# Kernel tuning notes

Hardware: AMD Instinct MI355X
Metric: run time of the kernel (lower is better)

## Reference

```python
import jax, jax.numpy as jnp
import numpy as np

B, N, F = 512, 2048, 64
T = 4            # number of atom types
H1, H2 = 64, 32  # hidden widths; final layer outputs 1 (per-atom energy)


def setup_inputs() -> dict:
    key = jax.random.key(0)
    ks = jax.random.split(key, 8)
    x = jax.random.normal(ks[0], (B, N, F), dtype=jnp.float32)
    atomic_numbers = jax.random.randint(ks[1], (N,), 0, T)
    s = 0.05
    # Per-type MLP parameters, stacked over the type axis (torch Linear layout: [out, in]).
    w0 = jax.random.normal(ks[2], (T, H1, F), dtype=jnp.float32) * s
    b0 = jax.random.normal(ks[3], (T, H1), dtype=jnp.float32) * s
    w1 = jax.random.normal(ks[4], (T, H2, H1), dtype=jnp.float32) * s
    b1 = jax.random.normal(ks[5], (T, H2), dtype=jnp.float32) * s
    w2 = jax.random.normal(ks[6], (T, 1, H2), dtype=jnp.float32) * s
    b2 = jax.random.normal(ks[7], (T, 1), dtype=jnp.float32) * s
    return {"x": x, "atomic_numbers": atomic_numbers,
            "w0": w0, "b0": b0, "w1": w1, "b1": b1, "w2": w2, "b2": b2}


def reference(x, atomic_numbers, w0, b0, w1, b1, w2, b2):
    # Behler-Parrinello: route each atom through the MLP of its atom type,
    # then sum per-atom energies over atoms.  The torch version gathers atoms
    # by type, runs each type's MLP, and scatters back; here we evaluate all
    # T type-MLPs batched over the type axis and select with a one-hot mask
    # (identical math, jit-friendly, no data-dependent shapes).
    onehot = jax.nn.one_hot(atomic_numbers, w0.shape[0], dtype=x.dtype)  # [N, T]
    h = jax.nn.silu(jnp.einsum('bnf,thf->tbnh', x, w0) + b0[:, None, None, :])   # [T,B,N,H1]
    h = jax.nn.silu(jnp.einsum('tbnh,tgh->tbng', h, w1) + b1[:, None, None, :])  # [T,B,N,H2]
    e = jnp.einsum('tbng,tog->tbno', h, w2) + b2[:, None, None, :]               # [T,B,N,1]
    e = e[..., 0]                                                                # [T,B,N]
    per_atom = jnp.einsum('tbn,nt->bn', e, onehot)  # select the matching type per atom
    return per_atom.sum(axis=-1)                    # [B]
```

## Files before the change

### kernel.cpp

```cpp
#include <hip/hip_runtime.h>
#include <hip/hip_bf16.h>


#define B_ 512
#define N_ 2048
#define F_ 64
#define T_ 4
#define H1_ 64
#define H2_ 32

#define BT 16
#define WAVES 4
#define NPW 32
#define NCHUNK (WAVES * NPW)

typedef __attribute__((ext_vector_type(8))) short bf16x8;
typedef __attribute__((ext_vector_type(4))) short bf16x4;
typedef __attribute__((ext_vector_type(4))) float f32x4;

__device__ inline float silu_f(float v) {
    return v * __builtin_amdgcn_rcpf(1.0f + __expf(-v));
}

__device__ inline bf16x8 pack8(float4 a, float4 b) {
    union { __hip_bfloat162 h[4]; bf16x8 v; } u;
    u.h[0] = __float22bfloat162_rn({a.x, a.y});
    u.h[1] = __float22bfloat162_rn({a.z, a.w});
    u.h[2] = __float22bfloat162_rn({b.x, b.y});
    u.h[3] = __float22bfloat162_rn({b.z, b.w});
    return u.v;
}

__global__ __launch_bounds__(256, 4) void bpnn_kernel(
    const float* __restrict__ x, const int* __restrict__ an,
    const float* __restrict__ w0, const float* __restrict__ b0,
    const float* __restrict__ w1, const float* __restrict__ b1,
    const float* __restrict__ w2, const float* __restrict__ b2,
    float* __restrict__ out)
{
    __shared__ __align__(16) __hip_bfloat16 w0s[T_][H1_][72];
    __shared__ __align__(16) __hip_bfloat16 w1s[T_][H2_][72];
    __shared__ __align__(16) __hip_bfloat16 h1s[WAVES][BT][68];
    __shared__ __align__(16) __hip_bfloat16 w2s[T_][H2_];
    __shared__ __align__(16) __hip_bfloat16 b0s[T_][H1_];
    __shared__ __align__(16) __hip_bfloat16 b1s[T_][H2_];
    __shared__ __align__(16) int ans[NCHUNK];

    const int tid = threadIdx.x;

    for (int i = tid; i < T_ * H1_ * F_; i += 256)
        w0s[i >> 12][(i >> 6) & 63][i & 63] = __float2bfloat16(w0[i]);
    for (int i = tid; i < T_ * H2_ * H1_; i += 256)
        w1s[i >> 11][(i >> 6) & 31][i & 63] = __float2bfloat16(w1[i]);
    if (tid < T_ * H2_) w2s[tid >> 5][tid & 31] = __float2bfloat16(w2[tid]);
    if (tid < T_ * H1_) b0s[tid >> 6][tid & 63] = __float2bfloat16(b0[tid]);
    if (tid < T_ * H2_) b1s[tid >> 5][tid & 31] = __float2bfloat16(b1[tid]);
    if (tid < NCHUNK)   ans[tid] = an[blockIdx.x * NCHUNK + tid];
    const float b2r0 = b2[0], b2r1 = b2[1], b2r2 = b2[2], b2r3 = b2[3];
    __syncthreads();

    const int wave = tid >> 6;
    const int lane = tid & 63;
    const int lr   = lane & 15;
    const int q    = lane >> 4;
    const int b0i  = blockIdx.y * BT;
    const float* xrow = x + ((size_t)(b0i + lr) * N_) * F_ + q * 8;

    float esum[4] = {0.f, 0.f, 0.f, 0.f};
    float bsum = 0.f;

    for (int it = 0; it < NPW; ++it) {
        const int nloc = wave * NPW + it;
        int t = ans[nloc];
        t = __builtin_amdgcn_readfirstlane(t);

        const float4* xp = reinterpret_cast<const float4*>(xrow + (size_t)(blockIdx.x * NCHUNK + nloc) * F_);
        float4 xa = xp[0], xb = xp[1], xc = xp[8], xd = xp[9];
        bf16x8 a0 = pack8(xa, xb);
        bf16x8 a1 = pack8(xc, xd);

        f32x4 acc[4] = {{0,0,0,0},{0,0,0,0},{0,0,0,0},{0,0,0,0}};
#pragma unroll
        for (int nt = 0; nt < 4; ++nt) {
            bf16x8 bw0 = *reinterpret_cast<const bf16x8*>(&w0s[t][nt * 16 + lr][q * 8]);
            acc[nt] = __builtin_amdgcn_mfma_f32_16x16x32_bf16(a0, bw0, acc[nt], 0, 0, 0);
            bf16x8 bw1 = *reinterpret_cast<const bf16x8*>(&w0s[t][nt * 16 + lr][32 + q * 8]);
            acc[nt] = __builtin_amdgcn_mfma_f32_16x16x32_bf16(a1, bw1, acc[nt], 0, 0, 0);
        }
#pragma unroll
        for (int nt = 0; nt < 4; ++nt) {
            float bias = __bfloat162float(b0s[t][nt * 16 + lr]);
#pragma unroll
            for (int r = 0; r < 4; ++r) {
                float v = silu_f(acc[nt][r] + bias);
                h1s[wave][q * 4 + r][nt * 16 + lr] = __float2bfloat16(v);
            }
        }
        __builtin_amdgcn_wave_barrier();

        bf16x4 lo0 = *reinterpret_cast<const bf16x4*>(&h1s[wave][lr][q * 8]);
        bf16x4 hi0 = *reinterpret_cast<const bf16x4*>(&h1s[wave][lr][q * 8 + 4]);
        bf16x4 lo1 = *reinterpret_cast<const bf16x4*>(&h1s[wave][lr][32 + q * 8]);
        bf16x4 hi1 = *reinterpret_cast<const bf16x4*>(&h1s[wave][lr][32 + q * 8 + 4]);
        bf16x8 h1a0 = __builtin_shufflevector(lo0, hi0, 0, 1, 2, 3, 4, 5, 6, 7);
        bf16x8 h1a1 = __builtin_shufflevector(lo1, hi1, 0, 1, 2, 3, 4, 5, 6, 7);
        __builtin_amdgcn_wave_barrier();

        f32x4 accB[2] = {{0,0,0,0},{0,0,0,0}};
#pragma unroll
        for (int nt = 0; nt < 2; ++nt) {
            bf16x8 bw0 = *reinterpret_cast<const bf16x8*>(&w1s[t][nt * 16 + lr][q * 8]);
            accB[nt] = __builtin_amdgcn_mfma_f32_16x16x32_bf16(h1a0, bw0, accB[nt], 0, 0, 0);
            bf16x8 bw1 = *reinterpret_cast<const bf16x8*>(&w1s[t][nt * 16 + lr][32 + q * 8]);
            accB[nt] = __builtin_amdgcn_mfma_f32_16x16x32_bf16(h1a1, bw1, accB[nt], 0, 0, 0);
        }
        float w2v0 = __bfloat162float(w2s[t][lr]);
        float w2v1 = __bfloat162float(w2s[t][16 + lr]);
        float bi0  = __bfloat162float(b1s[t][lr]);
        float bi1  = __bfloat162float(b1s[t][16 + lr]);
#pragma unroll
        for (int r = 0; r < 4; ++r) {
            float vA = silu_f(accB[0][r] + bi0);
            float vB = silu_f(accB[1][r] + bi1);
            esum[r] += vA * w2v0 + vB * w2v1;
        }
        bsum += (t == 0) ? b2r0 : (t == 1) ? b2r1 : (t == 2) ? b2r2 : b2r3;
    }

#pragma unroll
    for (int m = 1; m < 16; m <<= 1) {
#pragma unroll
        for (int r = 0; r < 4; ++r) esum[r] += __shfl_xor(esum[r], m, 16);
    }

    __syncthreads();
    float* red = reinterpret_cast<float*>(ans);
    if (tid < BT) red[tid] = 0.0f;
    __syncthreads();
    if (lr == 0) {
#pragma unroll
        for (int r = 0; r < 4; ++r)
            atomicAdd(&red[q * 4 + r], esum[r] + bsum);
    }
    __syncthreads();
    if (tid < BT) atomicAdd(&out[b0i + tid], red[tid]);
}

extern "C" void kernel_launch(void* const* d_in, const int* in_sizes, int n_in,
                              void* d_out, int out_size, void* d_ws, size_t ws_size,
                              hipStream_t stream) {
    const float* x  = (const float*)d_in[0];
    const int*   an = (const int*)d_in[1];
    const float* w0 = (const float*)d_in[2];
    const float* b0 = (const float*)d_in[3];
    const float* w1 = (const float*)d_in[4];
    const float* b1 = (const float*)d_in[5];
    const float* w2 = (const float*)d_in[6];
    const float* b2 = (const float*)d_in[7];
    float* out = (float*)d_out;

    hipMemsetAsync(out, 0, B_ * sizeof(float), stream);
    dim3 grid(N_ / NCHUNK, B_ / BT);
    bpnn_kernel<<<grid, 256, 0, stream>>>(x, an, w0, b0, w1, b1, w2, b2, out);
}
```

Measured before the change: 398.3 us.

## Transpose MFMA operands, prefetch next atom's x row, and simplify reduction

Swaps MFMA operand roles so weights are the A operand and x/h1 are B. Each lane's outputs then sit in a contiguous row, which allows vectorized bf16x4 stores of h1 and vector bias loads, and reduces the final reduction to two cross-quad shuffles. The kernel software-prefetches the next atom's x row and type index into registers, replacing the LDS staging of atom types. It also lowers the launch-bounds occupancy hint from 4 to 2, which frees registers but may reduce waves per CU.

```diff
diff --git a/kernel.cpp b/kernel.cpp
--- a/kernel.cpp
+++ b/kernel.cpp
@@ -31,7 +31,14 @@
     return u.v;
 }
 
-__global__ __launch_bounds__(256, 4) void bpnn_kernel(
+__device__ inline bf16x4 pack4(float a, float b, float c, float d) {
+    union { __hip_bfloat162 h[2]; bf16x4 v; } u;
+    u.h[0] = __float22bfloat162_rn({a, b});
+    u.h[1] = __float22bfloat162_rn({c, d});
+    return u.v;
+}
+
+__global__ __launch_bounds__(256, 2) void bpnn_kernel(
     const float* __restrict__ x, const int* __restrict__ an,
     const float* __restrict__ w0, const float* __restrict__ b0,
     const float* __restrict__ w1, const float* __restrict__ b1,
@@ -40,11 +47,10 @@
 {
     __shared__ __align__(16) __hip_bfloat16 w0s[T_][H1_][72];
     __shared__ __align__(16) __hip_bfloat16 w1s[T_][H2_][72];
-    __shared__ __align__(16) __hip_bfloat16 h1s[WAVES][BT][68];
+    __shared__ __align__(16) __hip_bfloat16 trb[WAVES][BT][72];
     __shared__ __align__(16) __hip_bfloat16 w2s[T_][H2_];
     __shared__ __align__(16) __hip_bfloat16 b0s[T_][H1_];
     __shared__ __align__(16) __hip_bfloat16 b1s[T_][H2_];
-    __shared__ __align__(16) int ans[NCHUNK];
 
     const int tid = threadIdx.x;
 
@@ -55,7 +61,6 @@
     if (tid < T_ * H2_) w2s[tid >> 5][tid & 31] = __float2bfloat16(w2[tid]);
     if (tid < T_ * H1_) b0s[tid >> 6][tid & 63] = __float2bfloat16(b0[tid]);
     if (tid < T_ * H2_) b1s[tid >> 5][tid & 31] = __float2bfloat16(b1[tid]);
-    if (tid < NCHUNK)   ans[tid] = an[blockIdx.x * NCHUNK + tid];
     const float b2r0 = b2[0], b2r1 = b2[1], b2r2 = b2[2], b2r3 = b2[3];
     __syncthreads();
 
@@ -64,84 +69,89 @@
     const int lr   = lane & 15;
     const int q    = lane >> 4;
     const int b0i  = blockIdx.y * BT;
-    const float* xrow = x + ((size_t)(b0i + lr) * N_) * F_ + q * 8;
+    const int gn0  = blockIdx.x * NCHUNK + wave * NPW;
 
-    float esum[4] = {0.f, 0.f, 0.f, 0.f};
+    const float4* xp = reinterpret_cast<const float4*>(
+        x + (size_t)(b0i + lr) * N_ * F_ + (size_t)gn0 * F_ + q * 8);
+
+    __hip_bfloat16* trbw = &trb[wave][lr][0];
+
+    float esum = 0.f;
     float bsum = 0.f;
 
+    float4 pa = xp[0], pb = xp[1], pc = xp[8], pd = xp[9];
+    int tpre = an[gn0];
+
     for (int it = 0; it < NPW; ++it) {
-        const int nloc = wave * NPW + it;
-        int t = ans[nloc];
-        t = __builtin_amdgcn_readfirstlane(t);
+        const int t = __builtin_amdgcn_readfirstlane(tpre);
+        float4 xa = pa, xb = pb, xc = pc, xd = pd;
 
-        const float4* xp = reinterpret_cast<const float4*>(xrow + (size_t)(blockIdx.x * NCHUNK + nloc) * F_);
-        float4 xa = xp[0], xb = xp[1], xc = xp[8], xd = xp[9];
-        bf16x8 a0 = pack8(xa, xb);
-        bf16x8 a1 = pack8(xc, xd);
+        {
+            const int nx = (it + 1 < NPW) ? (it + 1) : (NPW - 1);
+            const int o = nx * 16;
+            pa = xp[o]; pb = xp[o + 1]; pc = xp[o + 8]; pd = xp[o + 9];
+            tpre = an[gn0 + nx];
+        }
+
+        bf16x8 xb0 = pack8(xa, xb);
+        bf16x8 xb1 = pack8(xc, xd);
+
+        const __hip_bfloat16* w0t = &w0s[t][0][0];
+        const __hip_bfloat16* w1t = &w1s[t][0][0];
+        const int rowoff = lr * 72 + q * 8;
 
         f32x4 acc[4] = {{0,0,0,0},{0,0,0,0},{0,0,0,0},{0,0,0,0}};
 #pragma unroll
         for (int nt = 0; nt < 4; ++nt) {
-            bf16x8 bw0 = *reinterpret_cast<const bf16x8*>(&w0s[t][nt * 16 + lr][q * 8]);
-            acc[nt] = __builtin_amdgcn_mfma_f32_16x16x32_bf16(a0, bw0, acc[nt], 0, 0, 0);
-            bf16x8 bw1 = *reinterpret_cast<const bf16x8*>(&w0s[t][nt * 16 + lr][32 + q * 8]);
-            acc[nt] = __builtin_amdgcn_mfma_f32_16x16x32_bf16(a1, bw1, acc[nt], 0, 0, 0);
+            bf16x8 aw0 = *reinterpret_cast<const bf16x8*>(w0t + nt * 16 * 72 + rowoff);
+            acc[nt] = __builtin_amdgcn_mfma_f32_16x16x32_bf16(aw0, xb0, acc[nt], 0, 0, 0);
+            bf16x8 aw1 = *reinterpret_cast<const bf16x8*>(w0t + nt * 16 * 72 + rowoff + 32);
+            acc[nt] = __builtin_amdgcn_mfma_f32_16x16x32_bf16(aw1, xb1, acc[nt], 0, 0, 0);
         }
 #pragma unroll
         for (int nt = 0; nt < 4; ++nt) {
-            float bias = __bfloat162float(b0s[t][nt * 16 + lr]);
-#pragma unroll
-            for (int r = 0; r < 4; ++r) {
-                float v = silu_f(acc[nt][r] + bias);
-                h1s[wave][q * 4 + r][nt * 16 + lr] = __float2bfloat16(v);
-            }
+            bf16x4 bb = *reinterpret_cast<const bf16x4*>(&b0s[t][nt * 16 + q * 4]);
+            float v0 = silu_f(acc[nt][0] + __bfloat162float(((__hip_bfloat16*)&bb)[0]));
+            float v1 = silu_f(acc[nt][1] + __bfloat162float(((__hip_bfloat16*)&bb)[1]));
+            float v2 = silu_f(acc[nt][2] + __bfloat162float(((__hip_bfloat16*)&bb)[2]));
+            float v3 = silu_f(acc[nt][3] + __bfloat162float(((__hip_bfloat16*)&bb)[3]));
+            *reinterpret_cast<bf16x4*>(trbw + nt * 16 + q * 4) = pack4(v0, v1, v2, v3);
         }
         __builtin_amdgcn_wave_barrier();
 
-        bf16x4 lo0 = *reinterpret_cast<const bf16x4*>(&h1s[wave][lr][q * 8]);
-        bf16x4 hi0 = *reinterpret_cast<const bf16x4*>(&h1s[wave][lr][q * 8 + 4]);
-        bf16x4 lo1 = *reinterpret_cast<const bf16x4*>(&h1s[wave][lr][32 + q * 8]);
-        bf16x4 hi1 = *reinterpret_cast<const bf16x4*>(&h1s[wave][lr][32 + q * 8 + 4]);
-        bf16x8 h1a0 = __builtin_shufflevector(lo0, hi0, 0, 1, 2, 3, 4, 5, 6, 7);
-        bf16x8 h1a1 = __builtin_shufflevector(lo1, hi1, 0, 1, 2, 3, 4, 5, 6, 7);
+        bf16x8 hb0 = *reinterpret_cast<const bf16x8*>(trbw + q * 8);
+        bf16x8 hb1 = *reinterpret_cast<const bf16x8*>(trbw + 32 + q * 8);
         __builtin_amdgcn_wave_barrier();
 
         f32x4 accB[2] = {{0,0,0,0},{0,0,0,0}};
 #pragma unroll
-        for (int nt = 0; nt < 2; ++nt) {
-            bf16x8 bw0 = *reinterpret_cast<const bf16x8*>(&w1s[t][nt * 16 + lr][q * 8]);
-            accB[nt] = __builtin_amdgcn_mfma_f32_16x16x32_bf16(h1a0, bw0, accB[nt], 0, 0, 0);
-            bf16x8 bw1 = *reinterpret_cast<const bf16x8*>(&w1s[t][nt * 16 + lr][32 + q * 8]);
-            accB[nt] = __builtin_amdgcn_mfma_f32_16x16x32_bf16(h1a1, bw1, accB[nt], 0, 0, 0);
+        for (int mt = 0; mt < 2; ++mt) {
+            bf16x8 aw0 = *reinterpret_cast<const bf16x8*>(w1t + mt * 16 * 72 + rowoff);
+            accB[mt] = __builtin_amdgcn_mfma_f32_16x16x32_bf16(aw0, hb0, accB[mt], 0, 0, 0);
+            bf16x8 aw1 = *reinterpret_cast<const bf16x8*>(w1t + mt * 16 * 72 + rowoff + 32);
+            accB[mt] = __builtin_amdgcn_mfma_f32_16x16x32_bf16(aw1, hb1, accB[mt], 0, 0, 0);
         }
-        float w2v0 = __bfloat162float(w2s[t][lr]);
-        float w2v1 = __bfloat162float(w2s[t][16 + lr]);
-        float bi0  = __bfloat162float(b1s[t][lr]);
-        float bi1  = __bfloat162float(b1s[t][16 + lr]);
 #pragma unroll
-        for (int r = 0; r < 4; ++r) {
-            float vA = silu_f(accB[0][r] + bi0);
-            float vB = silu_f(accB[1][r] + bi1);
-            esum[r] += vA * w2v0 + vB * w2v1;
+        for (int mt = 0; mt < 2; ++mt) {
+            bf16x4 bb = *reinterpret_cast<const bf16x4*>(&b1s[t][mt * 16 + q * 4]);
+            bf16x4 ww = *reinterpret_cast<const bf16x4*>(&w2s[t][mt * 16 + q * 4]);
+#pragma unroll
+            for (int r = 0; r < 4; ++r) {
+                float v = silu_f(accB[mt][r] + __bfloat162float(((__hip_bfloat16*)&bb)[r]));
+                esum += v * __bfloat162float(((__hip_bfloat16*)&ww)[r]);
+            }
         }
         bsum += (t == 0) ? b2r0 : (t == 1) ? b2r1 : (t == 2) ? b2r2 : b2r3;
     }
 
-#pragma unroll
-    for (int m = 1; m < 16; m <<= 1) {
-#pragma unroll
-        for (int r = 0; r < 4; ++r) esum[r] += __shfl_xor(esum[r], m, 16);
-    }
+    esum += __shfl_xor(esum, 16);
+    esum += __shfl_xor(esum, 32);
 
     __syncthreads();
-    float* red = reinterpret_cast<float*>(ans);
+    float* red = reinterpret_cast<float*>(&w0s[0][0][0]);
     if (tid < BT) red[tid] = 0.0f;
     __syncthreads();
-    if (lr == 0) {
-#pragma unroll
-        for (int r = 0; r < 4; ++r)
-            atomicAdd(&red[q * 4 + r], esum[r] + bsum);
-    }
+    if (q == 0) atomicAdd(&red[lr], esum + bsum);
     __syncthreads();
     if (tid < BT) atomicAdd(&out[b0i + tid], red[tid]);
 }
```

After: 395.5 us. About the same (-0.7%).
